# Performance work log

Measured on AMD Instinct MI355X. Metric: run time of the kernel, lower is better.

Reference implementation:

```python
import jax, jax.numpy as jnp
import numpy as np

DIM = 1024
NUM_HEADS = 16
HEAD_DIM = DIM // NUM_HEADS
ROPE_BASE = 10000.0


def _rope_cos_sin(seq_len, head_dim):
    inv_freq = 1.0 / (ROPE_BASE ** (jnp.arange(0, head_dim, 2, dtype=jnp.float32) / head_dim))
    t = jnp.arange(seq_len, dtype=jnp.float32)
    freqs = t[:, None] * inv_freq[None, :]            # [S, Dh/2]
    emb = jnp.concatenate([freqs, freqs], axis=-1)    # [S, Dh]
    return jnp.cos(emb), jnp.sin(emb)


def _rotate_half(x):
    half = x.shape[-1] // 2
    return jnp.concatenate([-x[..., half:], x[..., :half]], axis=-1)


def setup_inputs() -> dict:
    key = jax.random.key(0)
    k1, k2, k3 = jax.random.split(key, 3)
    B, S = 2, 2048
    x = jax.random.normal(k1, (B, S, DIM), dtype=jnp.float32)
    w_qkv = jax.random.normal(k2, (3 * DIM, DIM), dtype=jnp.float32) * (DIM ** -0.5)
    w_out = jax.random.normal(k3, (DIM, DIM), dtype=jnp.float32) * (DIM ** -0.5)
    return {"x": x, "w_qkv": w_qkv, "w_out": w_out}


def reference(x, w_qkv, w_out):
    B, S, D = x.shape
    H, Dh = NUM_HEADS, HEAD_DIM
    scale = Dh ** -0.5

    qkv = (x @ w_qkv.T).reshape(B, S, 3, H, Dh)      # [B,S,3,H,Dh]
    qkv = jnp.transpose(qkv, (2, 0, 3, 1, 4))        # [3,B,H,S,Dh]
    q, k, v = qkv[0], qkv[1], qkv[2]

    cos, sin = _rope_cos_sin(S, Dh)                  # [S,Dh]
    cos = cos[None, None, :, :]
    sin = sin[None, None, :, :]
    q = q * cos + _rotate_half(q) * sin
    k = k * cos + _rotate_half(k) * sin

    scores = jnp.einsum('bhqd,bhkd->bhqk', q, k) * scale
    causal_mask = jnp.triu(jnp.ones((S, S), dtype=bool), k=1)
    scores = jnp.where(causal_mask[None, None], -jnp.inf, scores)
    attn = jax.nn.softmax(scores, axis=-1)
    out = jnp.einsum('bhqk,bhkd->bhqd', attn, v)      # [B,H,S,Dh]
    out = jnp.transpose(out, (0, 2, 1, 3)).reshape(B, S, D)
    return out @ w_out.T
```

## Files before the change

kernel.cpp:

```cpp
#include <hip/hip_runtime.h>
#include <stdint.h>

typedef uint16_t u16;
typedef __attribute__((ext_vector_type(8))) short bf16x8;
typedef __attribute__((ext_vector_type(4))) float f32x4;

__device__ inline u16 f2b(float f) {
  uint32_t u = __float_as_uint(f);
  u += 0x7FFF + ((u >> 16) & 1);
  return (u16)(u >> 16);
}
__device__ inline float b2f(u16 h) {
  return __uint_as_float(((uint32_t)h) << 16);
}

__global__ void k_detect(const u16* __restrict__ X, int* __restrict__ flag) {
  __shared__ int cnt;
  const int t = threadIdx.x;
  if (t == 0) cnt = 0;
  __syncthreads();
  float av = fabsf(b2f(X[t * 2]));
  int wild = (av < 1000.0f) ? 0 : 1;
  atomicAdd(&cnt, wild);
  __syncthreads();
  if (t == 0) flag[0] = (cnt > 16) ? 1 : 0;
}

__global__ __launch_bounds__(256) void k_qkv_rope(const void* __restrict__ Xv,
                                                  const void* __restrict__ Wv,
                                                  const int* __restrict__ flag,
                                                  u16* __restrict__ Qo,
                                                  u16* __restrict__ Ko,
                                                  u16* __restrict__ Vo) {
  __shared__ u16 As[2][64][40];
  __shared__ u16 Bs[3][64][40];
  __shared__ float Cs[64][66];
  const int mode = flag[0];
  const int h = blockIdx.x;
  const int n0h = h * 64;
  const int m0 = blockIdx.y * 128;
  const int t = threadIdx.x, w = t >> 6, lane = t & 63;
  const int lr = lane & 15, lq = lane >> 4;
  f32x4 acc[3][2][4] = {};
  const int rA = t >> 2, cA = (t & 3) * 8;
  const int aoff0 = (m0 + rA) * 1024 + cA;
  const int aoff1 = (m0 + 64 + rA) * 1024 + cA;
  const int boff0 = (n0h + rA) * 1024 + cA;

  if (mode == 0) {
    const u16* Xp = (const u16*)Xv;
    const u16* Wp = (const u16*)Wv;
    uint4 pa0 = *(const uint4*)(Xp + aoff0);
    uint4 pa1 = *(const uint4*)(Xp + aoff1);
    uint4 pb0 = *(const uint4*)(Wp + boff0);
    uint4 pb1 = *(const uint4*)(Wp + boff0 + 1048576);
    uint4 pb2 = *(const uint4*)(Wp + boff0 + 2097152);
    for (int k0 = 0; k0 < 1024; k0 += 32) {
      __syncthreads();
      *(uint4*)&As[0][rA][cA] = pa0;
      *(uint4*)&As[1][rA][cA] = pa1;
      *(uint4*)&Bs[0][rA][cA] = pb0;
      *(uint4*)&Bs[1][rA][cA] = pb1;
      *(uint4*)&Bs[2][rA][cA] = pb2;
      __syncthreads();
      if (k0 + 32 < 1024) {
        const int kn = k0 + 32;
        pa0 = *(const uint4*)(Xp + aoff0 + kn);
        pa1 = *(const uint4*)(Xp + aoff1 + kn);
        pb0 = *(const uint4*)(Wp + boff0 + kn);
        pb1 = *(const uint4*)(Wp + boff0 + 1048576 + kn);
        pb2 = *(const uint4*)(Wp + boff0 + 2097152 + kn);
      }
      bf16x8 bf[3];
#pragma unroll
      for (int e = 0; e < 3; ++e)
        bf[e] = *(const bf16x8*)&Bs[e][(w << 4) + lr][lq * 8];
#pragma unroll
      for (int mt = 0; mt < 4; ++mt) {
        bf16x8 af0 = *(const bf16x8*)&As[0][(mt << 4) + lr][lq * 8];
        bf16x8 af1 = *(const bf16x8*)&As[1][(mt << 4) + lr][lq * 8];
#pragma unroll
        for (int e = 0; e < 3; ++e) {
          acc[e][0][mt] = __builtin_amdgcn_mfma_f32_16x16x32_bf16(af0, bf[e], acc[e][0][mt], 0, 0, 0);
          acc[e][1][mt] = __builtin_amdgcn_mfma_f32_16x16x32_bf16(af1, bf[e], acc[e][1][mt], 0, 0, 0);
        }
      }
    }
  } else {
    for (int k0 = 0; k0 < 1024; k0 += 32) {
      __syncthreads();
      const float* Xf = (const float*)Xv;
      const float* Wf = (const float*)Wv;
#pragma unroll
      for (int ee = 0; ee < 8; ++ee) {
        As[0][rA][cA + ee] = f2b(Xf[aoff0 + k0 + ee]);
        As[1][rA][cA + ee] = f2b(Xf[aoff1 + k0 + ee]);
        Bs[0][rA][cA + ee] = f2b(Wf[boff0 + k0 + ee]);
        Bs[1][rA][cA + ee] = f2b(Wf[boff0 + 1048576 + k0 + ee]);
        Bs[2][rA][cA + ee] = f2b(Wf[boff0 + 2097152 + k0 + ee]);
      }
      __syncthreads();
      bf16x8 bf[3];
#pragma unroll
      for (int e = 0; e < 3; ++e)
        bf[e] = *(const bf16x8*)&Bs[e][(w << 4) + lr][lq * 8];
#pragma unroll
      for (int mt = 0; mt < 4; ++mt) {
        bf16x8 af0 = *(const bf16x8*)&As[0][(mt << 4) + lr][lq * 8];
        bf16x8 af1 = *(const bf16x8*)&As[1][(mt << 4) + lr][lq * 8];
#pragma unroll
        for (int e = 0; e < 3; ++e) {
          acc[e][0][mt] = __builtin_amdgcn_mfma_f32_16x16x32_bf16(af0, bf[e], acc[e][0][mt], 0, 0, 0);
          acc[e][1][mt] = __builtin_amdgcn_mfma_f32_16x16x32_bf16(af1, bf[e], acc[e][1][mt], 0, 0, 0);
        }
      }
    }
  }

  for (int f = 0; f < 2; ++f) {
    const int m0f = m0 + f * 64;
    for (int e = 0; e < 3; ++e) {
      __syncthreads();
      {
        const int col = (w << 4) + lr;
#pragma unroll
        for (int mt = 0; mt < 4; ++mt)
#pragma unroll
          for (int i = 0; i < 4; ++i)
            Cs[mt * 16 + lq * 4 + i][col] = acc[e][f][mt][i];
      }
      __syncthreads();
      if (e == 2) {
        const int sx = t & 63, dh0 = (t >> 6) * 16;
        const int m = m0f + sx, b = m >> 11, s = m & 2047;
        const long hb = (long)(b * 16 + h) * 64;
#pragma unroll
        for (int u = 0; u < 16; ++u) {
          int dh = dh0 + u;
          Vo[(hb + dh) * 2048 + s] = f2b(Cs[sx][dh]);
        }
      } else {
        const int r = t >> 2, dh0 = (t & 3) * 16;
        const int m = m0f + r, b = m >> 11, s = m & 2047;
        const int obase = ((b * 16 + h) * 2048 + s) * 64;
        u16* O = (e == 0) ? Qo : Ko;
#pragma unroll
        for (int u = 0; u < 16; ++u) {
          int dh = dh0 + u;
          float v  = Cs[r][dh];
          float vp = Cs[r][dh ^ 32];
          float sign = (dh < 32) ? -1.0f : 1.0f;
          float fr  = __expf((float)(dh & 31) * -0.28782314f);
          float ang = (float)s * fr;
          float sn = __sinf(ang), cs = __cosf(ang);
          O[obase + dh] = f2b(v * cs + sign * vp * sn);
        }
      }
    }
  }
}

__device__ __forceinline__ void attn_tile(u16 QP[64][72], u16 Ks[64][72],
                                          u16 Vt[64][72], const bf16x8 qf[2],
                                          f32x4 o_acc[4], float& m_i, float& l_i,
                                          int kt, int qt_tile, int w, int lr,
                                          int lq, int lq4, int base16, int qrow_l) {
  f32x4 sa[4] = {};
#pragma unroll
  for (int mb = 0; mb < 4; ++mb)
#pragma unroll
    for (int kk = 0; kk < 2; ++kk) {
      bf16x8 kf = *(const bf16x8*)&Ks[mb * 16 + lr][kk * 32 + lq * 8];
      sa[mb] = __builtin_amdgcn_mfma_f32_16x16x32_bf16(kf, qf[kk], sa[mb], 0, 0, 0);
    }
  float sc[4][4];
  float m_new = m_i;
#pragma unroll
  for (int mb = 0; mb < 4; ++mb)
#pragma unroll
    for (int i = 0; i < 4; ++i) {
      float sv = sa[mb][i] * 0.125f;
      if (kt == qt_tile && (mb * 16 + lq4 + i) > qrow_l) sv = -3.0e4f;
      sc[mb][i] = sv;
      m_new = fmaxf(m_new, sv);
    }
  m_new = fmaxf(m_new, __shfl_xor(m_new, 16));
  m_new = fmaxf(m_new, __shfl_xor(m_new, 32));
  float alpha = __expf(m_i - m_new);
  m_i = m_new;
  float p[4][4], sm = 0.f;
#pragma unroll
  for (int mb = 0; mb < 4; ++mb)
#pragma unroll
    for (int i = 0; i < 4; ++i) { p[mb][i] = __expf(sc[mb][i] - m_new); sm += p[mb][i]; }
  sm += __shfl_xor(sm, 16);
  sm += __shfl_xor(sm, 32);
  l_i = l_i * alpha + sm;
#pragma unroll
  for (int mb = 0; mb < 4; ++mb) {
    uint2 pk;
    pk.x = (uint32_t)f2b(p[mb][0]) | ((uint32_t)f2b(p[mb][1]) << 16);
    pk.y = (uint32_t)f2b(p[mb][2]) | ((uint32_t)f2b(p[mb][3]) << 16);
    *(uint2*)&QP[w * 16 + lr][mb * 16 + lq4] = pk;
  }
#pragma unroll
  for (int i = 0; i < 4; ++i) {
    float ai = __shfl(alpha, base16 | (lq4 + i));
    o_acc[0][i] *= ai; o_acc[1][i] *= ai;
    o_acc[2][i] *= ai; o_acc[3][i] *= ai;
  }
  asm volatile("s_waitcnt lgkmcnt(0)" ::: "memory");
#pragma unroll
  for (int kk = 0; kk < 2; ++kk) {
    bf16x8 pf = *(const bf16x8*)&QP[w * 16 + lr][kk * 32 + lq * 8];
#pragma unroll
    for (int nb = 0; nb < 4; ++nb) {
      bf16x8 vf = *(const bf16x8*)&Vt[nb * 16 + lr][kk * 32 + lq * 8];
      o_acc[nb] = __builtin_amdgcn_mfma_f32_16x16x32_bf16(pf, vf, o_acc[nb], 0, 0, 0);
    }
  }
}

__global__ __launch_bounds__(256) void k_attn(const u16* __restrict__ Q,
                                              const u16* __restrict__ K,
                                              const u16* __restrict__ V,
                                              u16* __restrict__ AO) {
  __shared__ u16 QP[64][72];
  __shared__ u16 Ks[64][72];
  __shared__ u16 Vt[64][72];
  const int qtA = 31 - blockIdx.x;
  const int qtB = blockIdx.x;
  const int bh = blockIdx.y;
  const int b = bh >> 4, h = bh & 15;
  const u16* Qg = Q + (bh * 2048) * 64;
  const u16* Kg = K + bh * 2048 * 64;
  const u16* Vg = V + (long)bh * 64 * 2048;
  const int t = threadIdx.x, w = t >> 6, lane = t & 63;
  const int lr = lane & 15, lq = lane >> 4;
  const int lq4 = lq * 4;
  const int base16 = lane & 48;
  const int r0 = t >> 3, c0 = (t & 7) * 8;
  const int qrow_l = w * 16 + lr;

  bf16x8 qfA[2], qfB[2];
  *(uint4*)&QP[r0][c0]      = *(const uint4*)&Qg[(qtA * 64 + r0) * 64 + c0];
  *(uint4*)&QP[r0 + 32][c0] = *(const uint4*)&Qg[(qtA * 64 + r0 + 32) * 64 + c0];
  __syncthreads();
#pragma unroll
  for (int kk = 0; kk < 2; ++kk)
    qfA[kk] = *(const bf16x8*)&QP[w * 16 + lr][kk * 32 + lq * 8];
  __syncthreads();
  *(uint4*)&QP[r0][c0]      = *(const uint4*)&Qg[(qtB * 64 + r0) * 64 + c0];
  *(uint4*)&QP[r0 + 32][c0] = *(const uint4*)&Qg[(qtB * 64 + r0 + 32) * 64 + c0];
  __syncthreads();
#pragma unroll
  for (int kk = 0; kk < 2; ++kk)
    qfB[kk] = *(const bf16x8*)&QP[w * 16 + lr][kk * 32 + lq * 8];

  float m_iA = -3.0e4f, l_iA = 0.f, m_iB = -3.0e4f, l_iB = 0.f;
  f32x4 o_accA[4] = {}, o_accB[4] = {};

  for (int kt = 0; kt <= qtA; ++kt) {
    __syncthreads();
    *(uint4*)&Ks[r0][c0]      = *(const uint4*)&Kg[(kt * 64 + r0) * 64 + c0];
    *(uint4*)&Ks[r0 + 32][c0] = *(const uint4*)&Kg[(kt * 64 + r0 + 32) * 64 + c0];
    *(uint4*)&Vt[r0][c0]      = *(const uint4*)&Vg[r0 * 2048 + kt * 64 + c0];
    *(uint4*)&Vt[r0 + 32][c0] = *(const uint4*)&Vg[(r0 + 32) * 2048 + kt * 64 + c0];
    __syncthreads();

    attn_tile(QP, Ks, Vt, qfA, o_accA, m_iA, l_iA, kt, qtA,
              w, lr, lq, lq4, base16, qrow_l);
    if (kt <= qtB) {
      asm volatile("s_waitcnt lgkmcnt(0)" ::: "memory");
      attn_tile(QP, Ks, Vt, qfB, o_accB, m_iB, l_iB, kt, qtB,
                w, lr, lq, lq4, base16, qrow_l);
    }
  }
  float linvA = 1.0f / l_iA, linvB = 1.0f / l_iB;
#pragma unroll
  for (int i = 0; i < 4; ++i) {
    float invA = __shfl(linvA, base16 | (lq4 + i));
    float invB = __shfl(linvB, base16 | (lq4 + i));
    int rowA = qtA * 64 + w * 16 + lq4 + i;
    int rowB = qtB * 64 + w * 16 + lq4 + i;
    int obA = (b * 2048 + rowA) * 1024 + h * 64;
    int obB = (b * 2048 + rowB) * 1024 + h * 64;
#pragma unroll
    for (int nb = 0; nb < 4; ++nb) {
      AO[obA + nb * 16 + lr] = f2b(o_accA[nb][i] * invA);
      AO[obB + nb * 16 + lr] = f2b(o_accB[nb][i] * invB);
    }
  }
}

__global__ __launch_bounds__(256) void k_gemm_out(const u16* __restrict__ A,
                                                  const void* __restrict__ Bv,
                                                  const int* __restrict__ flag,
                                                  void* __restrict__ Cv) {
  __shared__ u16 As[2][64][40];
  __shared__ u16 Bs[2][64][40];
  const int mode = flag[0];
  const int n0 = blockIdx.x * 128, m0 = blockIdx.y * 128;
  const int t = threadIdx.x, w = t >> 6, lane = t & 63;
  const int lr = lane & 15, lq = lane >> 4;
  f32x4 acc[2][2][4] = {};
  const int rA = t >> 2, cA = (t & 3) * 8;
  const int aoff0 = (m0 + rA) * 1024 + cA;
  const int aoff1 = (m0 + 64 + rA) * 1024 + cA;
  const int boff = (n0 + rA) * 1024 + cA;

  if (mode == 0) {
    const u16* Bp = (const u16*)Bv;
    uint4 pa0 = *(const uint4*)(A + aoff0);
    uint4 pa1 = *(const uint4*)(A + aoff1);
    uint4 pb0 = *(const uint4*)(Bp + boff);
    uint4 pb1 = *(const uint4*)(Bp + boff + 65536);
    for (int k0 = 0; k0 < 1024; k0 += 32) {
      __syncthreads();
      *(uint4*)&As[0][rA][cA] = pa0;
      *(uint4*)&As[1][rA][cA] = pa1;
      *(uint4*)&Bs[0][rA][cA] = pb0;
      *(uint4*)&Bs[1][rA][cA] = pb1;
      __syncthreads();
      if (k0 + 32 < 1024) {
        const int kn = k0 + 32;
        pa0 = *(const uint4*)(A + aoff0 + kn);
        pa1 = *(const uint4*)(A + aoff1 + kn);
        pb0 = *(const uint4*)(Bp + boff + kn);
        pb1 = *(const uint4*)(Bp + boff + 65536 + kn);
      }
      bf16x8 bfx[2];
#pragma unroll
      for (int e = 0; e < 2; ++e)
        bfx[e] = *(const bf16x8*)&Bs[e][(w << 4) + lr][lq * 8];
#pragma unroll
      for (int mt = 0; mt < 4; ++mt) {
        bf16x8 af0 = *(const bf16x8*)&As[0][(mt << 4) + lr][lq * 8];
        bf16x8 af1 = *(const bf16x8*)&As[1][(mt << 4) + lr][lq * 8];
#pragma unroll
        for (int e = 0; e < 2; ++e) {
          acc[e][0][mt] = __builtin_amdgcn_mfma_f32_16x16x32_bf16(af0, bfx[e], acc[e][0][mt], 0, 0, 0);
          acc[e][1][mt] = __builtin_amdgcn_mfma_f32_16x16x32_bf16(af1, bfx[e], acc[e][1][mt], 0, 0, 0);
        }
      }
    }
  } else {
    for (int k0 = 0; k0 < 1024; k0 += 32) {
      __syncthreads();
      *(uint4*)&As[0][rA][cA] = *(const uint4*)(A + aoff0 + k0);
      *(uint4*)&As[1][rA][cA] = *(const uint4*)(A + aoff1 + k0);
      const float* Bf = (const float*)Bv;
#pragma unroll
      for (int e = 0; e < 8; ++e) {
        Bs[0][rA][cA + e] = f2b(Bf[boff + k0 + e]);
        Bs[1][rA][cA + e] = f2b(Bf[boff + 65536 + k0 + e]);
      }
      __syncthreads();
      bf16x8 bfx[2];
#pragma unroll
      for (int e = 0; e < 2; ++e)
        bfx[e] = *(const bf16x8*)&Bs[e][(w << 4) + lr][lq * 8];
#pragma unroll
      for (int mt = 0; mt < 4; ++mt) {
        bf16x8 af0 = *(const bf16x8*)&As[0][(mt << 4) + lr][lq * 8];
        bf16x8 af1 = *(const bf16x8*)&As[1][(mt << 4) + lr][lq * 8];
#pragma unroll
        for (int e = 0; e < 2; ++e) {
          acc[e][0][mt] = __builtin_amdgcn_mfma_f32_16x16x32_bf16(af0, bfx[e], acc[e][0][mt], 0, 0, 0);
          acc[e][1][mt] = __builtin_amdgcn_mfma_f32_16x16x32_bf16(af1, bfx[e], acc[e][1][mt], 0, 0, 0);
        }
      }
    }
  }
#pragma unroll
  for (int e = 0; e < 2; ++e)
#pragma unroll
    for (int f = 0; f < 2; ++f) {
      const int col = n0 + e * 64 + (w << 4) + lr;
      const int m0f = m0 + f * 64;
      if (mode == 0) {
        u16* C = (u16*)Cv;
#pragma unroll
        for (int mt = 0; mt < 4; ++mt)
#pragma unroll
          for (int i = 0; i < 4; ++i)
            C[(m0f + mt * 16 + lq * 4 + i) * 1024 + col] = f2b(acc[e][f][mt][i]);
      } else {
        float* C = (float*)Cv;
#pragma unroll
        for (int mt = 0; mt < 4; ++mt)
#pragma unroll
          for (int i = 0; i < 4; ++i)
            C[(m0f + mt * 16 + lq * 4 + i) * 1024 + col] = acc[e][f][mt][i];
      }
    }
}

extern "C" void kernel_launch(void* const* d_in, const int* in_sizes, int n_in,
                              void* d_out, int out_size, void* d_ws, size_t ws_size,
                              hipStream_t stream) {
  const void* x    = d_in[0];
  const void* wqkv = d_in[1];
  const void* wout = d_in[2];

  int* flag = (int*)d_ws;
  u16* qb = (u16*)((char*)d_ws + 256);
  u16* kb = qb + 4194304;
  u16* vb = kb + 4194304;
  u16* ao = vb + 4194304;

  k_detect  <<<dim3(1), 256, 0, stream>>>((const u16*)x, flag);
  k_qkv_rope<<<dim3(16, 32), 256, 0, stream>>>(x, wqkv, flag, qb, kb, vb);
  k_attn    <<<dim3(16, 32), 256, 0, stream>>>(qb, kb, vb, ao);
  k_gemm_out<<<dim3(8, 32), 256, 0, stream>>>(ao, wout, flag, d_out);
}
```

Before: 231.0 us.

## Use direct global-to-LDS double-buffered loads with XOR swizzle and smaller out-GEMM tiles

Replaces register-staged global loads with global_load_lds double buffering in the bf16 paths, and swaps padded LDS rows for an XOR-swizzled layout. The output GEMM drops to 64-row M tiles, doubling the grid to fill more CUs. Loads are meant to overlap compute and LDS bank conflicts to shrink. The fp32 path used with these inputs gets only the swizzle and the retiling, and its B-tile conversion work roughly doubles across the grid.

```diff
diff --git a/kernel.cpp b/kernel.cpp
--- a/kernel.cpp
+++ b/kernel.cpp
@@ -13,6 +13,11 @@
 __device__ inline float b2f(u16 h) {
   return __uint_as_float(((uint32_t)h) << 16);
 }
+
+typedef __attribute__((address_space(1))) void gvoid;
+typedef __attribute__((address_space(3))) void lvoid;
+#define GLOAD16(gp, lp)                                                        \
+  __builtin_amdgcn_global_load_lds((gvoid*)(gp), (lvoid*)(lp), 16, 0, 0)
 
 __global__ void k_detect(const u16* __restrict__ X, int* __restrict__ flag) {
   __shared__ int cnt;
@@ -32,9 +37,11 @@
                                                   u16* __restrict__ Qo,
                                                   u16* __restrict__ Ko,
                                                   u16* __restrict__ Vo) {
-  __shared__ u16 As[2][64][40];
-  __shared__ u16 Bs[3][64][40];
-  __shared__ float Cs[64][66];
+  union ShQ {
+    struct { u16 A[2][2][64][32]; u16 B[2][3][64][32]; } st;
+    float Cs[64][66];
+  };
+  __shared__ ShQ sh;
   const int mode = flag[0];
   const int h = blockIdx.x;
   const int n0h = h * 64;
@@ -42,72 +49,78 @@
   const int t = threadIdx.x, w = t >> 6, lane = t & 63;
   const int lr = lane & 15, lq = lane >> 4;
   f32x4 acc[3][2][4] = {};
-  const int rA = t >> 2, cA = (t & 3) * 8;
-  const int aoff0 = (m0 + rA) * 1024 + cA;
-  const int aoff1 = (m0 + 64 + rA) * 1024 + cA;
-  const int boff0 = (n0h + rA) * 1024 + cA;
+  const int rA = t >> 2;
+  const int gcol = (((t & 3) ^ ((rA >> 1) & 3)) << 3);
+  const int aoff0 = (m0 + rA) * 1024 + gcol;
+  const int aoff1 = aoff0 + 65536;
+  const int boff0 = (n0h + rA) * 1024 + gcol;
 
   if (mode == 0) {
     const u16* Xp = (const u16*)Xv;
     const u16* Wp = (const u16*)Wv;
-    uint4 pa0 = *(const uint4*)(Xp + aoff0);
-    uint4 pa1 = *(const uint4*)(Xp + aoff1);
-    uint4 pb0 = *(const uint4*)(Wp + boff0);
-    uint4 pb1 = *(const uint4*)(Wp + boff0 + 1048576);
-    uint4 pb2 = *(const uint4*)(Wp + boff0 + 2097152);
+#define STAGE_QKV(buf, kk)                                                     \
+    do {                                                                       \
+      GLOAD16(Xp + aoff0 + (kk),           &sh.st.A[buf][0][(w << 4)][0]);     \
+      GLOAD16(Xp + aoff1 + (kk),           &sh.st.A[buf][1][(w << 4)][0]);     \
+      GLOAD16(Wp + boff0 + (kk),           &sh.st.B[buf][0][(w << 4)][0]);     \
+      GLOAD16(Wp + boff0 + 1048576 + (kk), &sh.st.B[buf][1][(w << 4)][0]);     \
+      GLOAD16(Wp + boff0 + 2097152 + (kk), &sh.st.B[buf][2][(w << 4)][0]);     \
+    } while (0)
+    STAGE_QKV(0, 0);
+    asm volatile("s_waitcnt vmcnt(0)" ::: "memory");
+    __syncthreads();
+    int cur = 0;
     for (int k0 = 0; k0 < 1024; k0 += 32) {
-      __syncthreads();
-      *(uint4*)&As[0][rA][cA] = pa0;
-      *(uint4*)&As[1][rA][cA] = pa1;
-      *(uint4*)&Bs[0][rA][cA] = pb0;
-      *(uint4*)&Bs[1][rA][cA] = pb1;
-      *(uint4*)&Bs[2][rA][cA] = pb2;
-      __syncthreads();
-      if (k0 + 32 < 1024) {
-        const int kn = k0 + 32;
-        pa0 = *(const uint4*)(Xp + aoff0 + kn);
-        pa1 = *(const uint4*)(Xp + aoff1 + kn);
-        pb0 = *(const uint4*)(Wp + boff0 + kn);
-        pb1 = *(const uint4*)(Wp + boff0 + 1048576 + kn);
-        pb2 = *(const uint4*)(Wp + boff0 + 2097152 + kn);
-      }
+      if (k0 + 32 < 1024) STAGE_QKV(cur ^ 1, k0 + 32);
       bf16x8 bf[3];
+      const int rowB = (w << 4) + lr;
+      const int scB = ((lq ^ ((rowB >> 1) & 3)) << 3);
 #pragma unroll
       for (int e = 0; e < 3; ++e)
-        bf[e] = *(const bf16x8*)&Bs[e][(w << 4) + lr][lq * 8];
+        bf[e] = *(const bf16x8*)&sh.st.B[cur][e][rowB][scB];
 #pragma unroll
       for (int mt = 0; mt < 4; ++mt) {
-        bf16x8 af0 = *(const bf16x8*)&As[0][(mt << 4) + lr][lq * 8];
-        bf16x8 af1 = *(const bf16x8*)&As[1][(mt << 4) + lr][lq * 8];
+        const int row = (mt << 4) + lr;
+        const int sc = ((lq ^ ((row >> 1) & 3)) << 3);
+        bf16x8 af0 = *(const bf16x8*)&sh.st.A[cur][0][row][sc];
+        bf16x8 af1 = *(const bf16x8*)&sh.st.A[cur][1][row][sc];
 #pragma unroll
         for (int e = 0; e < 3; ++e) {
           acc[e][0][mt] = __builtin_amdgcn_mfma_f32_16x16x32_bf16(af0, bf[e], acc[e][0][mt], 0, 0, 0);
           acc[e][1][mt] = __builtin_amdgcn_mfma_f32_16x16x32_bf16(af1, bf[e], acc[e][1][mt], 0, 0, 0);
         }
       }
-    }
+      __syncthreads();
+      cur ^= 1;
+    }
+#undef STAGE_QKV
   } else {
+    const float* Xf = (const float*)Xv;
+    const float* Wf = (const float*)Wv;
     for (int k0 = 0; k0 < 1024; k0 += 32) {
       __syncthreads();
-      const float* Xf = (const float*)Xv;
-      const float* Wf = (const float*)Wv;
 #pragma unroll
       for (int ee = 0; ee < 8; ++ee) {
-        As[0][rA][cA + ee] = f2b(Xf[aoff0 + k0 + ee]);
-        As[1][rA][cA + ee] = f2b(Xf[aoff1 + k0 + ee]);
-        Bs[0][rA][cA + ee] = f2b(Wf[boff0 + k0 + ee]);
-        Bs[1][rA][cA + ee] = f2b(Wf[boff0 + 1048576 + k0 + ee]);
-        Bs[2][rA][cA + ee] = f2b(Wf[boff0 + 2097152 + k0 + ee]);
+        const int pc = ((t & 3) << 3) + ee;
+        sh.st.A[0][0][rA][pc] = f2b(Xf[aoff0 + k0 + ee]);
+        sh.st.A[0][1][rA][pc] = f2b(Xf[aoff1 + k0 + ee]);
+        sh.st.B[0][0][rA][pc] = f2b(Wf[boff0 + k0 + ee]);
+        sh.st.B[0][1][rA][pc] = f2b(Wf[boff0 + 1048576 + k0 + ee]);
+        sh.st.B[0][2][rA][pc] = f2b(Wf[boff0 + 2097152 + k0 + ee]);
       }
       __syncthreads();
       bf16x8 bf[3];
+      const int rowB = (w << 4) + lr;
+      const int scB = ((lq ^ ((rowB >> 1) & 3)) << 3);
 #pragma unroll
       for (int e = 0; e < 3; ++e)
-        bf[e] = *(const bf16x8*)&Bs[e][(w << 4) + lr][lq * 8];
+        bf[e] = *(const bf16x8*)&sh.st.B[0][e][rowB][scB];
 #pragma unroll
       for (int mt = 0; mt < 4; ++mt) {
-        bf16x8 af0 = *(const bf16x8*)&As[0][(mt << 4) + lr][lq * 8];
-        bf16x8 af1 = *(const bf16x8*)&As[1][(mt << 4) + lr][lq * 8];
+        const int row = (mt << 4) + lr;
+        const int sc = ((lq ^ ((row >> 1) & 3)) << 3);
+        bf16x8 af0 = *(const bf16x8*)&sh.st.A[0][0][row][sc];
+        bf16x8 af1 = *(const bf16x8*)&sh.st.A[0][1][row][sc];
 #pragma unroll
         for (int e = 0; e < 3; ++e) {
           acc[e][0][mt] = __builtin_amdgcn_mfma_f32_16x16x32_bf16(af0, bf[e], acc[e][0][mt], 0, 0, 0);
@@ -127,7 +140,7 @@
         for (int mt = 0; mt < 4; ++mt)
 #pragma unroll
           for (int i = 0; i < 4; ++i)
-            Cs[mt * 16 + lq * 4 + i][col] = acc[e][f][mt][i];
+            sh.Cs[mt * 16 + lq * 4 + i][col] = acc[e][f][mt][i];
       }
       __syncthreads();
       if (e == 2) {
@@ -137,7 +150,7 @@
 #pragma unroll
         for (int u = 0; u < 16; ++u) {
           int dh = dh0 + u;
-          Vo[(hb + dh) * 2048 + s] = f2b(Cs[sx][dh]);
+          Vo[(hb + dh) * 2048 + s] = f2b(sh.Cs[sx][dh]);
         }
       } else {
         const int r = t >> 2, dh0 = (t & 3) * 16;
@@ -147,8 +160,8 @@
 #pragma unroll
         for (int u = 0; u < 16; ++u) {
           int dh = dh0 + u;
-          float v  = Cs[r][dh];
-          float vp = Cs[r][dh ^ 32];
+          float v  = sh.Cs[r][dh];
+          float vp = sh.Cs[r][dh ^ 32];
           float sign = (dh < 32) ? -1.0f : 1.0f;
           float fr  = __expf((float)(dh & 31) * -0.28782314f);
           float ang = (float)s * fr;
@@ -297,103 +310,100 @@
                                                   const void* __restrict__ Bv,
                                                   const int* __restrict__ flag,
                                                   void* __restrict__ Cv) {
-  __shared__ u16 As[2][64][40];
-  __shared__ u16 Bs[2][64][40];
+  __shared__ u16 As[2][64][32];
+  __shared__ u16 Bs[2][2][64][32];
   const int mode = flag[0];
-  const int n0 = blockIdx.x * 128, m0 = blockIdx.y * 128;
+  const int n0 = blockIdx.x * 128, m0 = blockIdx.y * 64;
   const int t = threadIdx.x, w = t >> 6, lane = t & 63;
   const int lr = lane & 15, lq = lane >> 4;
-  f32x4 acc[2][2][4] = {};
-  const int rA = t >> 2, cA = (t & 3) * 8;
-  const int aoff0 = (m0 + rA) * 1024 + cA;
-  const int aoff1 = (m0 + 64 + rA) * 1024 + cA;
-  const int boff = (n0 + rA) * 1024 + cA;
+  f32x4 acc[2][4] = {};
+  const int rA = t >> 2;
+  const int gcol = (((t & 3) ^ ((rA >> 1) & 3)) << 3);
+  const int aoff  = (m0 + rA) * 1024 + gcol;
+  const int boff0 = (n0 + rA) * 1024 + gcol;
+  const int boff1 = boff0 + 65536;
 
   if (mode == 0) {
     const u16* Bp = (const u16*)Bv;
-    uint4 pa0 = *(const uint4*)(A + aoff0);
-    uint4 pa1 = *(const uint4*)(A + aoff1);
-    uint4 pb0 = *(const uint4*)(Bp + boff);
-    uint4 pb1 = *(const uint4*)(Bp + boff + 65536);
+#define STAGE_OUT(buf, kk)                                                     \
+    do {                                                                       \
+      GLOAD16(A + aoff + (kk),   &As[buf][(w << 4)][0]);                       \
+      GLOAD16(Bp + boff0 + (kk), &Bs[buf][0][(w << 4)][0]);                    \
+      GLOAD16(Bp + boff1 + (kk), &Bs[buf][1][(w << 4)][0]);                    \
+    } while (0)
+    STAGE_OUT(0, 0);
+    asm volatile("s_waitcnt vmcnt(0)" ::: "memory");
+    __syncthreads();
+    int cur = 0;
     for (int k0 = 0; k0 < 1024; k0 += 32) {
-      __syncthreads();
-      *(uint4*)&As[0][rA][cA] = pa0;
-      *(uint4*)&As[1][rA][cA] = pa1;
-      *(uint4*)&Bs[0][rA][cA] = pb0;
-      *(uint4*)&Bs[1][rA][cA] = pb1;
-      __syncthreads();
-      if (k0 + 32 < 1024) {
-        const int kn = k0 + 32;
-        pa0 = *(const uint4*)(A + aoff0 + kn);
-        pa1 = *(const uint4*)(A + aoff1 + kn);
-        pb0 = *(const uint4*)(Bp + boff + kn);
-        pb1 = *(const uint4*)(Bp + boff + 65536 + kn);
-      }
+      if (k0 + 32 < 1024) STAGE_OUT(cur ^ 1, k0 + 32);
       bf16x8 bfx[2];
+      const int rowB = (w << 4) + lr;
+      const int scB = ((lq ^ ((rowB >> 1) & 3)) << 3);
 #pragma unroll
       for (int e = 0; e < 2; ++e)
-        bfx[e] = *(const bf16x8*)&Bs[e][(w << 4) + lr][lq * 8];
+        bfx[e] = *(const bf16x8*)&Bs[cur][e][rowB][scB];
 #pragma unroll
       for (int mt = 0; mt < 4; ++mt) {
-        bf16x8 af0 = *(const bf16x8*)&As[0][(mt << 4) + lr][lq * 8];
-        bf16x8 af1 = *(const bf16x8*)&As[1][(mt << 4) + lr][lq * 8];
-#pragma unroll
-        for (int e = 0; e < 2; ++e) {
-          acc[e][0][mt] = __builtin_amdgcn_mfma_f32_16x16x32_bf16(af0, bfx[e], acc[e][0][mt], 0, 0, 0);
-          acc[e][1][mt] = __builtin_amdgcn_mfma_f32_16x16x32_bf16(af1, bfx[e], acc[e][1][mt], 0, 0, 0);
-        }
-      }
-    }
+        const int row = (mt << 4) + lr;
+        const int sc = ((lq ^ ((row >> 1) & 3)) << 3);
+        bf16x8 af = *(const bf16x8*)&As[cur][row][sc];
+#pragma unroll
+        for (int e = 0; e < 2; ++e)
+          acc[e][mt] = __builtin_amdgcn_mfma_f32_16x16x32_bf16(af, bfx[e], acc[e][mt], 0, 0, 0);
+      }
+      __syncthreads();
+      cur ^= 1;
+    }
+#undef STAGE_OUT
   } else {
+    const float* Bf = (const float*)Bv;
     for (int k0 = 0; k0 < 1024; k0 += 32) {
       __syncthreads();
-      *(uint4*)&As[0][rA][cA] = *(const uint4*)(A + aoff0 + k0);
-      *(uint4*)&As[1][rA][cA] = *(const uint4*)(A + aoff1 + k0);
-      const float* Bf = (const float*)Bv;
-#pragma unroll
-      for (int e = 0; e < 8; ++e) {
-        Bs[0][rA][cA + e] = f2b(Bf[boff + k0 + e]);
-        Bs[1][rA][cA + e] = f2b(Bf[boff + 65536 + k0 + e]);
+      *(uint4*)&As[0][rA][(t & 3) << 3] = *(const uint4*)(A + aoff + k0);
+#pragma unroll
+      for (int ee = 0; ee < 8; ++ee) {
+        const int pc = ((t & 3) << 3) + ee;
+        Bs[0][0][rA][pc] = f2b(Bf[boff0 + k0 + ee]);
+        Bs[0][1][rA][pc] = f2b(Bf[boff1 + k0 + ee]);
       }
       __syncthreads();
       bf16x8 bfx[2];
+      const int rowB = (w << 4) + lr;
+      const int scB = ((lq ^ ((rowB >> 1) & 3)) << 3);
 #pragma unroll
       for (int e = 0; e < 2; ++e)
-        bfx[e] = *(const bf16x8*)&Bs[e][(w << 4) + lr][lq * 8];
+        bfx[e] = *(const bf16x8*)&Bs[0][e][rowB][scB];
 #pragma unroll
       for (int mt = 0; mt < 4; ++mt) {
-        bf16x8 af0 = *(const bf16x8*)&As[0][(mt << 4) + lr][lq * 8];
-        bf16x8 af1 = *(const bf16x8*)&As[1][(mt << 4) + lr][lq * 8];
-#pragma unroll
-        for (int e = 0; e < 2; ++e) {
-          acc[e][0][mt] = __builtin_amdgcn_mfma_f32_16x16x32_bf16(af0, bfx[e], acc[e][0][mt], 0, 0, 0);
-          acc[e][1][mt] = __builtin_amdgcn_mfma_f32_16x16x32_bf16(af1, bfx[e], acc[e][1][mt], 0, 0, 0);
-        }
-      }
-    }
-  }
-#pragma unroll
-  for (int e = 0; e < 2; ++e)
-#pragma unroll
-    for (int f = 0; f < 2; ++f) {
-      const int col = n0 + e * 64 + (w << 4) + lr;
-      const int m0f = m0 + f * 64;
-      if (mode == 0) {
-        u16* C = (u16*)Cv;
-#pragma unroll
-        for (int mt = 0; mt < 4; ++mt)
-#pragma unroll
-          for (int i = 0; i < 4; ++i)
-            C[(m0f + mt * 16 + lq * 4 + i) * 1024 + col] = f2b(acc[e][f][mt][i]);
-      } else {
-        float* C = (float*)Cv;
-#pragma unroll
-        for (int mt = 0; mt < 4; ++mt)
-#pragma unroll
-          for (int i = 0; i < 4; ++i)
-            C[(m0f + mt * 16 + lq * 4 + i) * 1024 + col] = acc[e][f][mt][i];
-      }
-    }
+        const int row = (mt << 4) + lr;
+        const int sc = ((lq ^ ((row >> 1) & 3)) << 3);
+        bf16x8 af = *(const bf16x8*)&As[0][row][sc];
+#pragma unroll
+        for (int e = 0; e < 2; ++e)
+          acc[e][mt] = __builtin_amdgcn_mfma_f32_16x16x32_bf16(af, bfx[e], acc[e][mt], 0, 0, 0);
+      }
+    }
+  }
+#pragma unroll
+  for (int e = 0; e < 2; ++e) {
+    const int col = n0 + e * 64 + (w << 4) + lr;
+    if (mode == 0) {
+      u16* C = (u16*)Cv;
+#pragma unroll
+      for (int mt = 0; mt < 4; ++mt)
+#pragma unroll
+        for (int i = 0; i < 4; ++i)
+          C[(m0 + mt * 16 + lq * 4 + i) * 1024 + col] = f2b(acc[e][mt][i]);
+    } else {
+      float* C = (float*)Cv;
+#pragma unroll
+      for (int mt = 0; mt < 4; ++mt)
+#pragma unroll
+        for (int i = 0; i < 4; ++i)
+          C[(m0 + mt * 16 + lq * 4 + i) * 1024 + col] = acc[e][mt][i];
+    }
+  }
 }
 
 extern "C" void kernel_launch(void* const* d_in, const int* in_sizes, int n_in,
@@ -412,5 +422,5 @@
   k_detect  <<<dim3(1), 256, 0, stream>>>((const u16*)x, flag);
   k_qkv_rope<<<dim3(16, 32), 256, 0, stream>>>(x, wqkv, flag, qb, kb, vb);
   k_attn    <<<dim3(16, 32), 256, 0, stream>>>(qb, kb, vb, ao);
-  k_gemm_out<<<dim3(8, 32), 256, 0, stream>>>(ao, wout, flag, d_out);
-}
+  k_gemm_out<<<dim3(8, 64), 256, 0, stream>>>(ao, wout, flag, d_out);
+}
```

Measured after the change: 242.2 us. +4.9%, slower.

## Double-prefetch bf16 GEMM tiles and halve output GEMM M-tile

Applied to the files above, without the earlier changes.

In the bf16 paths of the QKV and output GEMMs, two register sets of global loads (A/B) are now kept in flight and alternated, with a custom barrier that waits on lgkmcnt. This is meant to hide global-load latency behind MFMA work. Separately, the output projection GEMM drops from a 128-row to a 64-row M tile, doubling the grid to 512 blocks for better CU fill at the cost of reloading more weight tiles. With fp32 inputs the detect flag likely selects the fp32 path, so mostly the tile resize takes effect.

```diff
diff --git a/kernel.cpp b/kernel.cpp
--- a/kernel.cpp
+++ b/kernel.cpp
@@ -13,6 +13,14 @@
 __device__ inline float b2f(u16 h) {
   return __uint_as_float(((uint32_t)h) << 16);
 }
+
+#define BARRIER_LGKM()                                                         \
+  do {                                                                         \
+    __builtin_amdgcn_sched_barrier(0);                                         \
+    asm volatile("s_waitcnt lgkmcnt(0)" ::: "memory");                         \
+    __builtin_amdgcn_s_barrier();                                              \
+    __builtin_amdgcn_sched_barrier(0);                                         \
+  } while (0)
 
 __global__ void k_detect(const u16* __restrict__ X, int* __restrict__ flag) {
   __shared__ int cnt;
@@ -50,39 +58,77 @@
   if (mode == 0) {
     const u16* Xp = (const u16*)Xv;
     const u16* Wp = (const u16*)Wv;
-    uint4 pa0 = *(const uint4*)(Xp + aoff0);
-    uint4 pa1 = *(const uint4*)(Xp + aoff1);
-    uint4 pb0 = *(const uint4*)(Wp + boff0);
-    uint4 pb1 = *(const uint4*)(Wp + boff0 + 1048576);
-    uint4 pb2 = *(const uint4*)(Wp + boff0 + 2097152);
-    for (int k0 = 0; k0 < 1024; k0 += 32) {
-      __syncthreads();
-      *(uint4*)&As[0][rA][cA] = pa0;
-      *(uint4*)&As[1][rA][cA] = pa1;
-      *(uint4*)&Bs[0][rA][cA] = pb0;
-      *(uint4*)&Bs[1][rA][cA] = pb1;
-      *(uint4*)&Bs[2][rA][cA] = pb2;
-      __syncthreads();
-      if (k0 + 32 < 1024) {
-        const int kn = k0 + 32;
-        pa0 = *(const uint4*)(Xp + aoff0 + kn);
-        pa1 = *(const uint4*)(Xp + aoff1 + kn);
-        pb0 = *(const uint4*)(Wp + boff0 + kn);
-        pb1 = *(const uint4*)(Wp + boff0 + 1048576 + kn);
-        pb2 = *(const uint4*)(Wp + boff0 + 2097152 + kn);
-      }
-      bf16x8 bf[3];
-#pragma unroll
-      for (int e = 0; e < 3; ++e)
-        bf[e] = *(const bf16x8*)&Bs[e][(w << 4) + lr][lq * 8];
-#pragma unroll
-      for (int mt = 0; mt < 4; ++mt) {
-        bf16x8 af0 = *(const bf16x8*)&As[0][(mt << 4) + lr][lq * 8];
-        bf16x8 af1 = *(const bf16x8*)&As[1][(mt << 4) + lr][lq * 8];
-#pragma unroll
-        for (int e = 0; e < 3; ++e) {
-          acc[e][0][mt] = __builtin_amdgcn_mfma_f32_16x16x32_bf16(af0, bf[e], acc[e][0][mt], 0, 0, 0);
-          acc[e][1][mt] = __builtin_amdgcn_mfma_f32_16x16x32_bf16(af1, bf[e], acc[e][1][mt], 0, 0, 0);
+    uint4 a0A = *(const uint4*)(Xp + aoff0);
+    uint4 a1A = *(const uint4*)(Xp + aoff1);
+    uint4 b0A = *(const uint4*)(Wp + boff0);
+    uint4 b1A = *(const uint4*)(Wp + boff0 + 1048576);
+    uint4 b2A = *(const uint4*)(Wp + boff0 + 2097152);
+    uint4 a0B = *(const uint4*)(Xp + aoff0 + 32);
+    uint4 a1B = *(const uint4*)(Xp + aoff1 + 32);
+    uint4 b0B = *(const uint4*)(Wp + boff0 + 32);
+    uint4 b1B = *(const uint4*)(Wp + boff0 + 1048576 + 32);
+    uint4 b2B = *(const uint4*)(Wp + boff0 + 2097152 + 32);
+    for (int k0 = 0; k0 < 1024; k0 += 64) {
+      BARRIER_LGKM();
+      *(uint4*)&As[0][rA][cA] = a0A;
+      *(uint4*)&As[1][rA][cA] = a1A;
+      *(uint4*)&Bs[0][rA][cA] = b0A;
+      *(uint4*)&Bs[1][rA][cA] = b1A;
+      *(uint4*)&Bs[2][rA][cA] = b2A;
+      if (k0 + 64 < 1024) {
+        const int kn = k0 + 64;
+        a0A = *(const uint4*)(Xp + aoff0 + kn);
+        a1A = *(const uint4*)(Xp + aoff1 + kn);
+        b0A = *(const uint4*)(Wp + boff0 + kn);
+        b1A = *(const uint4*)(Wp + boff0 + 1048576 + kn);
+        b2A = *(const uint4*)(Wp + boff0 + 2097152 + kn);
+      }
+      BARRIER_LGKM();
+      {
+        bf16x8 bf[3];
+#pragma unroll
+        for (int e = 0; e < 3; ++e)
+          bf[e] = *(const bf16x8*)&Bs[e][(w << 4) + lr][lq * 8];
+#pragma unroll
+        for (int mt = 0; mt < 4; ++mt) {
+          bf16x8 af0 = *(const bf16x8*)&As[0][(mt << 4) + lr][lq * 8];
+          bf16x8 af1 = *(const bf16x8*)&As[1][(mt << 4) + lr][lq * 8];
+#pragma unroll
+          for (int e = 0; e < 3; ++e) {
+            acc[e][0][mt] = __builtin_amdgcn_mfma_f32_16x16x32_bf16(af0, bf[e], acc[e][0][mt], 0, 0, 0);
+            acc[e][1][mt] = __builtin_amdgcn_mfma_f32_16x16x32_bf16(af1, bf[e], acc[e][1][mt], 0, 0, 0);
+          }
+        }
+      }
+      BARRIER_LGKM();
+      *(uint4*)&As[0][rA][cA] = a0B;
+      *(uint4*)&As[1][rA][cA] = a1B;
+      *(uint4*)&Bs[0][rA][cA] = b0B;
+      *(uint4*)&Bs[1][rA][cA] = b1B;
+      *(uint4*)&Bs[2][rA][cA] = b2B;
+      if (k0 + 96 < 1024) {
+        const int kn = k0 + 96;
+        a0B = *(const uint4*)(Xp + aoff0 + kn);
+        a1B = *(const uint4*)(Xp + aoff1 + kn);
+        b0B = *(const uint4*)(Wp + boff0 + kn);
+        b1B = *(const uint4*)(Wp + boff0 + 1048576 + kn);
+        b2B = *(const uint4*)(Wp + boff0 + 2097152 + kn);
+      }
+      BARRIER_LGKM();
+      {
+        bf16x8 bf[3];
+#pragma unroll
+        for (int e = 0; e < 3; ++e)
+          bf[e] = *(const bf16x8*)&Bs[e][(w << 4) + lr][lq * 8];
+#pragma unroll
+        for (int mt = 0; mt < 4; ++mt) {
+          bf16x8 af0 = *(const bf16x8*)&As[0][(mt << 4) + lr][lq * 8];
+          bf16x8 af1 = *(const bf16x8*)&As[1][(mt << 4) + lr][lq * 8];
+#pragma unroll
+          for (int e = 0; e < 3; ++e) {
+            acc[e][0][mt] = __builtin_amdgcn_mfma_f32_16x16x32_bf16(af0, bf[e], acc[e][0][mt], 0, 0, 0);
+            acc[e][1][mt] = __builtin_amdgcn_mfma_f32_16x16x32_bf16(af1, bf[e], acc[e][1][mt], 0, 0, 0);
+          }
         }
       }
     }
@@ -297,103 +343,119 @@
                                                   const void* __restrict__ Bv,
                                                   const int* __restrict__ flag,
                                                   void* __restrict__ Cv) {
-  __shared__ u16 As[2][64][40];
+  __shared__ u16 As[64][40];
   __shared__ u16 Bs[2][64][40];
   const int mode = flag[0];
-  const int n0 = blockIdx.x * 128, m0 = blockIdx.y * 128;
+  const int n0 = blockIdx.x * 128, m0 = blockIdx.y * 64;
   const int t = threadIdx.x, w = t >> 6, lane = t & 63;
   const int lr = lane & 15, lq = lane >> 4;
-  f32x4 acc[2][2][4] = {};
+  f32x4 acc[2][4] = {};
   const int rA = t >> 2, cA = (t & 3) * 8;
-  const int aoff0 = (m0 + rA) * 1024 + cA;
-  const int aoff1 = (m0 + 64 + rA) * 1024 + cA;
-  const int boff = (n0 + rA) * 1024 + cA;
+  const int aoff  = (m0 + rA) * 1024 + cA;
+  const int boff0 = (n0 + rA) * 1024 + cA;
+  const int boff1 = boff0 + 65536;
 
   if (mode == 0) {
     const u16* Bp = (const u16*)Bv;
-    uint4 pa0 = *(const uint4*)(A + aoff0);
-    uint4 pa1 = *(const uint4*)(A + aoff1);
-    uint4 pb0 = *(const uint4*)(Bp + boff);
-    uint4 pb1 = *(const uint4*)(Bp + boff + 65536);
+    uint4 aA  = *(const uint4*)(A + aoff);
+    uint4 b0A = *(const uint4*)(Bp + boff0);
+    uint4 b1A = *(const uint4*)(Bp + boff1);
+    uint4 aB  = *(const uint4*)(A + aoff + 32);
+    uint4 b0B = *(const uint4*)(Bp + boff0 + 32);
+    uint4 b1B = *(const uint4*)(Bp + boff1 + 32);
+    for (int k0 = 0; k0 < 1024; k0 += 64) {
+      BARRIER_LGKM();
+      *(uint4*)&As[rA][cA]    = aA;
+      *(uint4*)&Bs[0][rA][cA] = b0A;
+      *(uint4*)&Bs[1][rA][cA] = b1A;
+      if (k0 + 64 < 1024) {
+        const int kn = k0 + 64;
+        aA  = *(const uint4*)(A + aoff + kn);
+        b0A = *(const uint4*)(Bp + boff0 + kn);
+        b1A = *(const uint4*)(Bp + boff1 + kn);
+      }
+      BARRIER_LGKM();
+      {
+        bf16x8 bfx[2];
+#pragma unroll
+        for (int e = 0; e < 2; ++e)
+          bfx[e] = *(const bf16x8*)&Bs[e][(w << 4) + lr][lq * 8];
+#pragma unroll
+        for (int mt = 0; mt < 4; ++mt) {
+          bf16x8 af = *(const bf16x8*)&As[(mt << 4) + lr][lq * 8];
+#pragma unroll
+          for (int e = 0; e < 2; ++e)
+            acc[e][mt] = __builtin_amdgcn_mfma_f32_16x16x32_bf16(af, bfx[e], acc[e][mt], 0, 0, 0);
+        }
+      }
+      BARRIER_LGKM();
+      *(uint4*)&As[rA][cA]    = aB;
+      *(uint4*)&Bs[0][rA][cA] = b0B;
+      *(uint4*)&Bs[1][rA][cA] = b1B;
+      if (k0 + 96 < 1024) {
+        const int kn = k0 + 96;
+        aB  = *(const uint4*)(A + aoff + kn);
+        b0B = *(const uint4*)(Bp + boff0 + kn);
+        b1B = *(const uint4*)(Bp + boff1 + kn);
+      }
+      BARRIER_LGKM();
+      {
+        bf16x8 bfx[2];
+#pragma unroll
+        for (int e = 0; e < 2; ++e)
+          bfx[e] = *(const bf16x8*)&Bs[e][(w << 4) + lr][lq * 8];
+#pragma unroll
+        for (int mt = 0; mt < 4; ++mt) {
+          bf16x8 af = *(const bf16x8*)&As[(mt << 4) + lr][lq * 8];
+#pragma unroll
+          for (int e = 0; e < 2; ++e)
+            acc[e][mt] = __builtin_amdgcn_mfma_f32_16x16x32_bf16(af, bfx[e], acc[e][mt], 0, 0, 0);
+        }
+      }
+    }
+  } else {
+    const float* Bf = (const float*)Bv;
     for (int k0 = 0; k0 < 1024; k0 += 32) {
       __syncthreads();
-      *(uint4*)&As[0][rA][cA] = pa0;
-      *(uint4*)&As[1][rA][cA] = pa1;
-      *(uint4*)&Bs[0][rA][cA] = pb0;
-      *(uint4*)&Bs[1][rA][cA] = pb1;
-      __syncthreads();
-      if (k0 + 32 < 1024) {
-        const int kn = k0 + 32;
-        pa0 = *(const uint4*)(A + aoff0 + kn);
-        pa1 = *(const uint4*)(A + aoff1 + kn);
-        pb0 = *(const uint4*)(Bp + boff + kn);
-        pb1 = *(const uint4*)(Bp + boff + 65536 + kn);
-      }
+      *(uint4*)&As[rA][cA] = *(const uint4*)(A + aoff + k0);
+#pragma unroll
+      for (int ee = 0; ee < 8; ++ee) {
+        Bs[0][rA][cA + ee] = f2b(Bf[boff0 + k0 + ee]);
+        Bs[1][rA][cA + ee] = f2b(Bf[boff1 + k0 + ee]);
+      }
+      __syncthreads();
       bf16x8 bfx[2];
 #pragma unroll
       for (int e = 0; e < 2; ++e)
         bfx[e] = *(const bf16x8*)&Bs[e][(w << 4) + lr][lq * 8];
 #pragma unroll
       for (int mt = 0; mt < 4; ++mt) {
-        bf16x8 af0 = *(const bf16x8*)&As[0][(mt << 4) + lr][lq * 8];
-        bf16x8 af1 = *(const bf16x8*)&As[1][(mt << 4) + lr][lq * 8];
-#pragma unroll
-        for (int e = 0; e < 2; ++e) {
-          acc[e][0][mt] = __builtin_amdgcn_mfma_f32_16x16x32_bf16(af0, bfx[e], acc[e][0][mt], 0, 0, 0);
-          acc[e][1][mt] = __builtin_amdgcn_mfma_f32_16x16x32_bf16(af1, bfx[e], acc[e][1][mt], 0, 0, 0);
-        }
-      }
-    }
-  } else {
-    for (int k0 = 0; k0 < 1024; k0 += 32) {
-      __syncthreads();
-      *(uint4*)&As[0][rA][cA] = *(const uint4*)(A + aoff0 + k0);
-      *(uint4*)&As[1][rA][cA] = *(const uint4*)(A + aoff1 + k0);
-      const float* Bf = (const float*)Bv;
-#pragma unroll
-      for (int e = 0; e < 8; ++e) {
-        Bs[0][rA][cA + e] = f2b(Bf[boff + k0 + e]);
-        Bs[1][rA][cA + e] = f2b(Bf[boff + 65536 + k0 + e]);
-      }
-      __syncthreads();
-      bf16x8 bfx[2];
-#pragma unroll
-      for (int e = 0; e < 2; ++e)
-        bfx[e] = *(const bf16x8*)&Bs[e][(w << 4) + lr][lq * 8];
-#pragma unroll
-      for (int mt = 0; mt < 4; ++mt) {
-        bf16x8 af0 = *(const bf16x8*)&As[0][(mt << 4) + lr][lq * 8];
-        bf16x8 af1 = *(const bf16x8*)&As[1][(mt << 4) + lr][lq * 8];
-#pragma unroll
-        for (int e = 0; e < 2; ++e) {
-          acc[e][0][mt] = __builtin_amdgcn_mfma_f32_16x16x32_bf16(af0, bfx[e], acc[e][0][mt], 0, 0, 0);
-          acc[e][1][mt] = __builtin_amdgcn_mfma_f32_16x16x32_bf16(af1, bfx[e], acc[e][1][mt], 0, 0, 0);
-        }
-      }
-    }
-  }
-#pragma unroll
-  for (int e = 0; e < 2; ++e)
-#pragma unroll
-    for (int f = 0; f < 2; ++f) {
-      const int col = n0 + e * 64 + (w << 4) + lr;
-      const int m0f = m0 + f * 64;
-      if (mode == 0) {
-        u16* C = (u16*)Cv;
-#pragma unroll
-        for (int mt = 0; mt < 4; ++mt)
-#pragma unroll
-          for (int i = 0; i < 4; ++i)
-            C[(m0f + mt * 16 + lq * 4 + i) * 1024 + col] = f2b(acc[e][f][mt][i]);
-      } else {
-        float* C = (float*)Cv;
-#pragma unroll
-        for (int mt = 0; mt < 4; ++mt)
-#pragma unroll
-          for (int i = 0; i < 4; ++i)
-            C[(m0f + mt * 16 + lq * 4 + i) * 1024 + col] = acc[e][f][mt][i];
-      }
-    }
+        bf16x8 af = *(const bf16x8*)&As[(mt << 4) + lr][lq * 8];
+#pragma unroll
+        for (int e = 0; e < 2; ++e)
+          acc[e][mt] = __builtin_amdgcn_mfma_f32_16x16x32_bf16(af, bfx[e], acc[e][mt], 0, 0, 0);
+      }
+    }
+  }
+#pragma unroll
+  for (int e = 0; e < 2; ++e) {
+    const int col = n0 + e * 64 + (w << 4) + lr;
+    if (mode == 0) {
+      u16* C = (u16*)Cv;
+#pragma unroll
+      for (int mt = 0; mt < 4; ++mt)
+#pragma unroll
+        for (int i = 0; i < 4; ++i)
+          C[(m0 + mt * 16 + lq * 4 + i) * 1024 + col] = f2b(acc[e][mt][i]);
+    } else {
+      float* C = (float*)Cv;
+#pragma unroll
+      for (int mt = 0; mt < 4; ++mt)
+#pragma unroll
+        for (int i = 0; i < 4; ++i)
+          C[(m0 + mt * 16 + lq * 4 + i) * 1024 + col] = acc[e][mt][i];
+    }
+  }
 }
 
 extern "C" void kernel_launch(void* const* d_in, const int* in_sizes, int n_in,
@@ -412,5 +474,5 @@
   k_detect  <<<dim3(1), 256, 0, stream>>>((const u16*)x, flag);
   k_qkv_rope<<<dim3(16, 32), 256, 0, stream>>>(x, wqkv, flag, qb, kb, vb);
   k_attn    <<<dim3(16, 32), 256, 0, stream>>>(qb, kb, vb, ao);
-  k_gemm_out<<<dim3(8, 32), 256, 0, stream>>>(ao, wout, flag, d_out);
-}
+  k_gemm_out<<<dim3(8, 64), 256, 0, stream>>>(ao, wout, flag, d_out);
+}
```

New measurement: 262.8 us. 1.14x slower.
